# Kernel tuning notes

Measured on AMD Instinct MI355X. Metric: run time of the kernel, lower is better.

The kernel has to match this reference:

```python
import jax, jax.numpy as jnp
import numpy as np

E, TOPK, D, F, FS = 16, 4, 2560, 1664, 3328
B, S = 1, 2048


def setup_inputs() -> dict:
    key = jax.random.key(0)
    ks = jax.random.split(key, 8)
    sc = lambda *sh: 1.0 / np.sqrt(sh[-2] if len(sh) > 1 else 1.0)
    return {
        "hidden_states": jax.random.normal(ks[0], (B, S, D), jnp.float32),
        "router_weight": jax.random.normal(ks[1], (E, D), jnp.float32) * (1.0 / np.sqrt(D)),
        "w_gate": jax.random.normal(ks[2], (E, D, F), jnp.float32) * (1.0 / np.sqrt(D)),
        "w_up": jax.random.normal(ks[3], (E, D, F), jnp.float32) * (1.0 / np.sqrt(D)),
        "w_down": jax.random.normal(ks[4], (E, F, D), jnp.float32) * (1.0 / np.sqrt(F)),
        "sw_gate": jax.random.normal(ks[5], (D, FS), jnp.float32) * (1.0 / np.sqrt(D)),
        "sw_up": jax.random.normal(ks[6], (D, FS), jnp.float32) * (1.0 / np.sqrt(D)),
        "sw_down": jax.random.normal(ks[7], (FS, D), jnp.float32) * (1.0 / np.sqrt(FS)),
    }


def reference(hidden_states, router_weight, w_gate, w_up, w_down, sw_gate, sw_up, sw_down):
    b, s, d = hidden_states.shape
    x = hidden_states.reshape(-1, d)  # [T, D]
    T = x.shape[0]

    # Router: linear -> softmax -> top-k -> renormalize (vLLM FusedMoE default)
    logits = x @ router_weight.T                      # [T, E]
    probs = jax.nn.softmax(logits, axis=-1)
    topk_w, topk_idx = jax.lax.top_k(probs, TOPK)     # [T, K]
    topk_w = topk_w / jnp.sum(topk_w, axis=-1, keepdims=True)
    combine = jnp.zeros((T, E), x.dtype).at[jnp.arange(T)[:, None], topk_idx].add(topk_w)  # [T, E]

    # Expert SiLU-gated MLPs (dense-dispatch reference for grouped GEMM)
    g = jnp.einsum('td,edf->tef', x, w_gate)          # [T, E, F]
    u = jnp.einsum('td,edf->tef', x, w_up)
    h = jax.nn.silu(g) * u
    y = jnp.einsum('tef,efd->ted', h, w_down)         # [T, E, D]
    sparse_out = jnp.einsum('ted,te->td', y, combine)

    # Shared expert: LlamaMLP with silu gate, no bias
    shared_out = (jax.nn.silu(x @ sw_gate) * (x @ sw_up)) @ sw_down

    return (sparse_out + shared_out).reshape(b, s, d)
```

## Files before the change

kernel.cpp:

```cpp
#include <hip/hip_runtime.h>
#include <hip/hip_bf16.h>
#include <stdint.h>

#define E_N 16
#define TOPK 4
#define DD 2560
#define FF 1664
#define FSS 3328
#define TT 2048

typedef __attribute__((ext_vector_type(8))) __bf16 bf16x8;
typedef __attribute__((ext_vector_type(4))) float f32x4;

__device__ __forceinline__ unsigned short f2bf(float f) {
  return __builtin_bit_cast(unsigned short, (__bf16)f);
}
__device__ __forceinline__ float bf2f(unsigned short u) {
  return __builtin_bit_cast(float, (unsigned int)u << 16);
}
__device__ __forceinline__ unsigned int pk2(float a, float b) {
  return (unsigned int)f2bf(a) | ((unsigned int)f2bf(b) << 16);
}

#define GLOAD16(g, l)                                                          \
  __builtin_amdgcn_global_load_lds(                                            \
      (const __attribute__((address_space(1))) void*)(g),                      \
      (__attribute__((address_space(3))) void*)(l), 16, 0, 0)

#define SBAR() __builtin_amdgcn_s_barrier()
#define VMW(N) asm volatile("s_waitcnt vmcnt(" #N ")" ::: "memory")

__device__ __forceinline__ void swz_block(int& bm, int& bn, int& bz) {
  int gx = gridDim.x, gy = gridDim.y;
  int nwg = gx * gy * gridDim.z;
  int flat = blockIdx.x + gx * (blockIdx.y + gy * blockIdx.z);
  if ((nwg & 7) == 0) flat = (flat & 7) * (nwg >> 3) + (flat >> 3);
  bm = flat % gx;
  int rest = flat / gx;
  bn = rest % gy;
  bz = rest / gy;
}

__global__ __launch_bounds__(256) void cvt_bf16_kernel(const float* __restrict__ in,
                                                       unsigned short* __restrict__ out) {
  size_t i = ((size_t)blockIdx.x * 256 + threadIdx.x) * 4;
  float4 v = *reinterpret_cast<const float4*>(in + i);
  ushort4 o;
  o.x = f2bf(v.x); o.y = f2bf(v.y); o.z = f2bf(v.z); o.w = f2bf(v.w);
  *reinterpret_cast<ushort4*>(out + i) = o;
}

__global__ __launch_bounds__(256) void tcvt_kernel(const float* __restrict__ in,
                                                   unsigned short* __restrict__ out,
                                                   int K, int N) {
  __shared__ float lds[64 * 65];
  int z = blockIdx.z;
  in += (size_t)z * K * N;
  out += (size_t)z * K * N;
  int k0 = blockIdx.x * 64, n0 = blockIdx.y * 64;
  int t = threadIdx.x;
#pragma unroll
  for (int j = 0; j < 4; ++j) {
    int idx = j * 256 + t;
    int r = idx >> 4, c = (idx & 15) * 4;
    float4 v = *reinterpret_cast<const float4*>(in + (size_t)(k0 + r) * N + n0 + c);
    lds[r * 65 + c] = v.x;
    lds[r * 65 + c + 1] = v.y;
    lds[r * 65 + c + 2] = v.z;
    lds[r * 65 + c + 3] = v.w;
  }
  __syncthreads();
#pragma unroll
  for (int j = 0; j < 2; ++j) {
    int idx = j * 256 + t;
    int n = idx >> 3, kg = (idx & 7) * 8;
    float a0 = lds[(kg + 0) * 65 + n], a1 = lds[(kg + 1) * 65 + n];
    float a2 = lds[(kg + 2) * 65 + n], a3 = lds[(kg + 3) * 65 + n];
    float a4 = lds[(kg + 4) * 65 + n], a5 = lds[(kg + 5) * 65 + n];
    float a6 = lds[(kg + 6) * 65 + n], a7 = lds[(kg + 7) * 65 + n];
    uint4 o{pk2(a0, a1), pk2(a2, a3), pk2(a4, a5), pk2(a6, a7)};
    *reinterpret_cast<uint4*>(out + (size_t)(n0 + n) * K + k0 + kg) = o;
  }
}

__global__ __launch_bounds__(256) void router_kernel(const float* __restrict__ x,
                                                     const float* __restrict__ rw,
                                                     int* __restrict__ cnt,
                                                     int* __restrict__ list,
                                                     float* __restrict__ tw) {
  int t = blockIdx.x;
  const float* xr = x + (size_t)t * DD;
  __shared__ float logits[E_N];
  int lane = threadIdx.x & 63, wid = threadIdx.x >> 6;
  for (int ee = 0; ee < 4; ++ee) {
    int e = wid * 4 + ee;
    const float* wr = rw + (size_t)e * DD;
    float p = 0.f;
    for (int d = lane; d < DD; d += 64) p += xr[d] * wr[d];
#pragma unroll
    for (int off = 32; off > 0; off >>= 1) p += __shfl_down(p, off);
    if (lane == 0) logits[e] = p;
  }
  __syncthreads();
  if (threadIdx.x == 0) {
    float mx = -1e30f;
    for (int e = 0; e < E_N; ++e) mx = fmaxf(mx, logits[e]);
    float pe[E_N];
    for (int e = 0; e < E_N; ++e) pe[e] = __expf(logits[e] - mx);
    int idx[TOPK]; float val[TOPK]; float s4 = 0.f;
    unsigned used = 0;
    for (int k = 0; k < TOPK; ++k) {
      int bi = 0; float bv = -1.f;
      for (int e = 0; e < E_N; ++e)
        if (!((used >> e) & 1) && pe[e] > bv) { bv = pe[e]; bi = e; }
      used |= 1u << bi; idx[k] = bi; val[k] = bv; s4 += bv;
    }
    float inv = 1.f / s4;
    for (int k = 0; k < TOPK; ++k) {
      int e2 = idx[k];
      int pos = atomicAdd(&cnt[e2], 1);
      list[e2 * TT + pos] = t * 4 + k;
      tw[t * 4 + k] = val[k] * inv;
    }
  }
}

template <int MODE, int SHIFT>
__device__ __forceinline__ void gemm256(
    const unsigned short* __restrict__ A0, const unsigned short* __restrict__ W0,
    void* __restrict__ O0, const int* lst, const float* __restrict__ tw,
    int M, int Kt, int Nt, int m0, int n0) {
  __shared__ __align__(16) unsigned short lds[2][32768];

  int tid = threadIdx.x, lane = tid & 63, w = tid >> 6;
  int wm = w >> 2, wn = w & 3;

  const unsigned short* pA[2];
  const unsigned short* pB[2];
#pragma unroll
  for (int j = 0; j < 2; ++j) {
    int id = j * 512 + tid;
    int row = id >> 2, c = id & 3;
    int cs = c ^ ((row >> 1) & 3);
    int ar = min(m0 + row, M - 1);
    int code = lst ? lst[ar] : ar;
    int arow = SHIFT ? (lst ? (code >> 2) : code) : code;
    pA[j] = A0 + (size_t)arow * Kt + cs * 8;
    int br = min(n0 + row, Nt - 1);
    pB[j] = W0 + (size_t)br * Kt + cs * 8;
  }

  auto stage = [&](int kt, int h, int buf) {
    int koff = kt * 64 + h * 32;
    unsigned short* dA = &lds[buf][h * 8192];
    unsigned short* dB = &lds[buf][16384 + h * 8192];
#pragma unroll
    for (int j = 0; j < 2; ++j) {
      GLOAD16(pA[j] + koff, dA + (j * 512 + tid) * 8);
      GLOAD16(pB[j] + koff, dB + (j * 512 + tid) * 8);
    }
  };

  int cg = lane >> 4;
  int aoff[8], boff[4];
#pragma unroll
  for (int mf = 0; mf < 8; ++mf) {
    int r = wm * 128 + mf * 16 + (lane & 15);
    aoff[mf] = r * 32 + ((cg ^ ((r >> 1) & 3)) * 8);
  }
#pragma unroll
  for (int nf = 0; nf < 4; ++nf) {
    int rb = wn * 64 + nf * 16 + (lane & 15);
    boff[nf] = 16384 + rb * 32 + ((cg ^ ((rb >> 1) & 3)) * 8);
  }

  f32x4 acc[8][4] = {};

  auto half_compute = [&](int buf, int h) {
    const unsigned short* L = &lds[buf][h * 8192];
    bf16x8 a[8], b[4];
#pragma unroll
    for (int nf = 0; nf < 4; ++nf)
      b[nf] = __builtin_bit_cast(bf16x8, *reinterpret_cast<const uint4*>(L + boff[nf]));
#pragma unroll
    for (int mf = 0; mf < 8; ++mf)
      a[mf] = __builtin_bit_cast(bf16x8, *reinterpret_cast<const uint4*>(L + aoff[mf]));
    __builtin_amdgcn_s_setprio(1);
#pragma unroll
    for (int mf = 0; mf < 8; ++mf)
#pragma unroll
      for (int nf = 0; nf < 4; ++nf)
        acc[mf][nf] = __builtin_amdgcn_mfma_f32_16x16x32_bf16(a[mf], b[nf], acc[mf][nf], 0, 0, 0);
    __builtin_amdgcn_s_setprio(0);
  };

  int nk = Kt / 64;
  stage(0, 0, 0);
  stage(0, 1, 0);
  stage(1, 0, 1);
  for (int kt = 0; kt < nk; ++kt) {
    int buf = kt & 1;
    if (kt + 1 < nk) { VMW(8); } else { VMW(4); }
    SBAR();
    if (kt + 1 < nk) stage(kt + 1, 1, buf ^ 1);
    half_compute(buf, 0);
    if (kt + 1 < nk) { VMW(8); } else { VMW(0); }
    SBAR();
    if (kt + 2 < nk) stage(kt + 2, 0, buf);
    half_compute(buf, 1);
  }

#pragma unroll
  for (int mf = 0; mf < 8; ++mf) {
#pragma unroll
    for (int q = 0; q < 4; ++q) {
      int lr = wm * 128 + mf * 16 + (lane >> 4) * 4 + q;
      int grow = m0 + lr;
      if (grow < M) {
        int code = lst ? lst[grow] : grow;
        int col = n0 + wn * 64 + (lane & 15);
        if (MODE == 0) {
          unsigned short* Op = (unsigned short*)O0 + (size_t)code * Nt + col;
#pragma unroll
          for (int nf = 0; nf < 4; ++nf)
            if (col + nf * 16 < Nt) Op[nf * 16] = f2bf(acc[mf][nf][q]);
        } else {
          float scale = tw ? tw[code] : 1.f;
          float* Op = (float*)O0 + (size_t)code * Nt + col;
#pragma unroll
          for (int nf = 0; nf < 4; ++nf)
            if (col + nf * 16 < Nt) Op[nf * 16] = acc[mf][nf][q] * scale;
        }
      }
    }
  }
}

__global__ __launch_bounds__(512, 1) void gu256_kernel(
    const unsigned short* __restrict__ Xb,
    const unsigned short* __restrict__ WgT, const unsigned short* __restrict__ WuT,
    const unsigned short* __restrict__ SgT, const unsigned short* __restrict__ SuT,
    unsigned short* __restrict__ Gx, unsigned short* __restrict__ Ux,
    unsigned short* __restrict__ Gs, unsigned short* __restrict__ Us,
    const int* __restrict__ list, const int* __restrict__ cnt) {
  int bm, bn, z;
  swz_block(bm, bn, z);
  bool up = z >= 17;
  int ze = up ? z - 17 : z;
  const unsigned short* W0;
  unsigned short* O0;
  const int* lst = nullptr;
  int M, Nt;
  if (ze < E_N) {
    M = cnt[ze];
    lst = list + ze * TT;
    Nt = FF;
    W0 = (up ? WuT : WgT) + (size_t)ze * DD * FF;
    O0 = up ? Ux : Gx;
  } else {
    M = TT;
    Nt = FSS;
    W0 = up ? SuT : SgT;
    O0 = up ? Us : Gs;
  }
  int m0 = bm * 256, n0 = bn * 256;
  if (m0 >= M || n0 >= Nt) return;
  gemm256<0, 1>(Xb, W0, O0, lst, nullptr, M, DD, Nt, m0, n0);
}

__global__ __launch_bounds__(512, 1) void dn256_kernel(
    const unsigned short* __restrict__ Hx, const unsigned short* __restrict__ Hs,
    const unsigned short* __restrict__ WdT, const unsigned short* __restrict__ SdT,
    float* __restrict__ Y, float* __restrict__ Ys,
    const int* __restrict__ list, const int* __restrict__ cnt,
    const float* __restrict__ tw) {
  int bm, bn, z;
  swz_block(bm, bn, z);
  const unsigned short* A0;
  const unsigned short* W0;
  float* O0;
  const int* lst = nullptr;
  const float* sc = nullptr;
  int M, Kt;
  if (z < E_N) {
    M = cnt[z];
    lst = list + z * TT;
    Kt = FF;
    A0 = Hx;
    W0 = WdT + (size_t)z * FF * DD;
    O0 = Y;
    sc = tw;
  } else {
    M = TT;
    Kt = FSS;
    A0 = Hs;
    W0 = SdT;
    O0 = Ys;
  }
  int m0 = bm * 256, n0 = bn * 256;
  if (m0 >= M) return;
  gemm256<1, 0>(A0, W0, O0, lst, sc, M, Kt, DD, m0, n0);
}

__global__ __launch_bounds__(256) void h_kernel(const unsigned short* __restrict__ g,
                                                unsigned short* __restrict__ u) {
  size_t i = ((size_t)blockIdx.x * 256 + threadIdx.x) * 8;
  uint4 gv = *reinterpret_cast<const uint4*>(g + i);
  uint4 uv = *reinterpret_cast<const uint4*>(u + i);
  const unsigned int* gw = reinterpret_cast<const unsigned int*>(&gv);
  const unsigned int* uw = reinterpret_cast<const unsigned int*>(&uv);
  uint4 ov;
  unsigned int* ow = reinterpret_cast<unsigned int*>(&ov);
#pragma unroll
  for (int j = 0; j < 4; ++j) {
    float g0 = bf2f((unsigned short)(gw[j] & 0xffff));
    float g1 = bf2f((unsigned short)(gw[j] >> 16));
    float u0 = bf2f((unsigned short)(uw[j] & 0xffff));
    float u1 = bf2f((unsigned short)(uw[j] >> 16));
    float h0 = (g0 / (1.f + __expf(-g0))) * u0;
    float h1 = (g1 / (1.f + __expf(-g1))) * u1;
    ow[j] = pk2(h0, h1);
  }
  *reinterpret_cast<uint4*>(u + i) = ov;
}

__global__ __launch_bounds__(256) void combine_kernel(const float* __restrict__ Y,
                                                      const float* __restrict__ Ys,
                                                      float* __restrict__ out) {
  size_t i = ((size_t)blockIdx.x * 256 + threadIdx.x) * 4;
  size_t t = i / DD;
  int d = (int)(i % DD);
  float4 a = *reinterpret_cast<const float4*>(Ys + i);
#pragma unroll
  for (int k = 0; k < 4; ++k) {
    float4 v = *reinterpret_cast<const float4*>(Y + (t * 4 + k) * (size_t)DD + d);
    a.x += v.x; a.y += v.y; a.z += v.z; a.w += v.w;
  }
  *reinterpret_cast<float4*>(out + i) = a;
}

extern "C" void kernel_launch(void* const* d_in, const int* in_sizes, int n_in,
                              void* d_out, int out_size, void* d_ws, size_t ws_size,
                              hipStream_t stream) {
  const float* x  = (const float*)d_in[0];
  const float* rw = (const float*)d_in[1];
  const float* wg = (const float*)d_in[2];
  const float* wu = (const float*)d_in[3];
  const float* wd = (const float*)d_in[4];
  const float* sg = (const float*)d_in[5];
  const float* su = (const float*)d_in[6];
  const float* sd = (const float*)d_in[7];
  float* out = (float*)d_out;

  char* ws = (char*)d_ws;
  size_t off = 0;
  auto alloc = [&](size_t bytes) {
    off = (off + 255) & ~(size_t)255;
    void* p = ws + off;
    off += bytes;
    return p;
  };
  unsigned short* W1 = (unsigned short*)alloc((size_t)E_N * FF * DD * 2);
  unsigned short* W2 = (unsigned short*)alloc((size_t)E_N * FF * DD * 2);
  unsigned short* W3 = (unsigned short*)alloc((size_t)FSS * DD * 2);
  unsigned short* W4 = (unsigned short*)alloc((size_t)FSS * DD * 2);
  unsigned short* Xb = (unsigned short*)alloc((size_t)TT * DD * 2);
  unsigned short* Gx = (unsigned short*)alloc((size_t)4 * TT * FF * 2);
  unsigned short* Hx = (unsigned short*)alloc((size_t)4 * TT * FF * 2);
  unsigned short* Gs = (unsigned short*)alloc((size_t)TT * FSS * 2);
  unsigned short* Hs = (unsigned short*)alloc((size_t)TT * FSS * 2);
  float* Y  = (float*)alloc((size_t)4 * TT * DD * 4);
  float* Ys = (float*)alloc((size_t)TT * DD * 4);
  float* tw = (float*)alloc((size_t)4 * TT * 4);
  int* cnt  = (int*)alloc(E_N * 4);
  int* list = (int*)alloc((size_t)E_N * TT * 4);
  (void)ws_size; (void)in_sizes; (void)n_in; (void)out_size;

  hipMemsetAsync(cnt, 0, E_N * 4, stream);
  cvt_bf16_kernel<<<TT * DD / 4 / 256, 256, 0, stream>>>(x, Xb);
  router_kernel<<<TT, 256, 0, stream>>>(x, rw, cnt, list, tw);

  tcvt_kernel<<<dim3(DD / 64, FF / 64, E_N), 256, 0, stream>>>(wg, W1, DD, FF);
  tcvt_kernel<<<dim3(DD / 64, FF / 64, E_N), 256, 0, stream>>>(wu, W2, DD, FF);
  tcvt_kernel<<<dim3(DD / 64, FSS / 64, 1), 256, 0, stream>>>(sg, W3, DD, FSS);
  tcvt_kernel<<<dim3(DD / 64, FSS / 64, 1), 256, 0, stream>>>(su, W4, DD, FSS);

  gu256_kernel<<<dim3(TT / 256, (FSS + 255) / 256, 34), 512, 0, stream>>>(
      Xb, W1, W2, W3, W4, Gx, Hx, Gs, Hs, list, cnt);

  h_kernel<<<(size_t)4 * TT * FF / 8 / 256, 256, 0, stream>>>(Gx, Hx);
  h_kernel<<<(size_t)TT * FSS / 8 / 256, 256, 0, stream>>>(Gs, Hs);

  tcvt_kernel<<<dim3(FF / 64, DD / 64, E_N), 256, 0, stream>>>(wd, W1, FF, DD);
  tcvt_kernel<<<dim3(FSS / 64, DD / 64, 1), 256, 0, stream>>>(sd, W2, FSS, DD);

  dn256_kernel<<<dim3(TT / 256, DD / 256, 17), 512, 0, stream>>>(
      Hx, Hs, W1, W2, Y, Ys, list, cnt, tw);

  combine_kernel<<<TT * DD / 4 / 256, 256, 0, stream>>>(Y, Ys, out);
}
```

Baseline: 1.265 ms.

## Rework GEMM main loop into triple-buffered K=32 stages with split phases

Replaces the double-buffered K=64 LDS pipeline with a three-slot ring of K=32 tiles, prefetching two stages ahead. Each K step is split into two M-halves whose global loads are issued between the LDS reads and the MFMA burst. The goal is deeper latency hiding with smaller per-stage LDS use, at the cost of more barriers per K step and different wait-count logic. The grid y dimension is also changed from a ceiling division to an exact FSS/256, which gives the same value here.

```diff
diff --git a/kernel.cpp b/kernel.cpp
--- a/kernel.cpp
+++ b/kernel.cpp
@@ -126,117 +126,115 @@
 }
 
 template <int MODE, int SHIFT>
-__device__ __forceinline__ void gemm256(
+__device__ __forceinline__ void gemm8(
     const unsigned short* __restrict__ A0, const unsigned short* __restrict__ W0,
     void* __restrict__ O0, const int* lst, const float* __restrict__ tw,
     int M, int Kt, int Nt, int m0, int n0) {
-  __shared__ __align__(16) unsigned short lds[2][32768];
+  __shared__ __align__(16) unsigned short lds[3][16384];
 
   int tid = threadIdx.x, lane = tid & 63, w = tid >> 6;
   int wm = w >> 2, wn = w & 3;
 
+  int scs = (tid & 3) ^ ((tid >> 3) & 3);
   const unsigned short* pA[2];
   const unsigned short* pB[2];
 #pragma unroll
-  for (int j = 0; j < 2; ++j) {
-    int id = j * 512 + tid;
-    int row = id >> 2, c = id & 3;
-    int cs = c ^ ((row >> 1) & 3);
+  for (int h = 0; h < 2; ++h) {
+    int row = h * 128 + (tid >> 2);
     int ar = min(m0 + row, M - 1);
     int code = lst ? lst[ar] : ar;
     int arow = SHIFT ? (lst ? (code >> 2) : code) : code;
-    pA[j] = A0 + (size_t)arow * Kt + cs * 8;
+    pA[h] = A0 + (size_t)arow * Kt + scs * 8;
     int br = min(n0 + row, Nt - 1);
-    pB[j] = W0 + (size_t)br * Kt + cs * 8;
-  }
-
-  auto stage = [&](int kt, int h, int buf) {
-    int koff = kt * 64 + h * 32;
-    unsigned short* dA = &lds[buf][h * 8192];
-    unsigned short* dB = &lds[buf][16384 + h * 8192];
-#pragma unroll
-    for (int j = 0; j < 2; ++j) {
-      GLOAD16(pA[j] + koff, dA + (j * 512 + tid) * 8);
-      GLOAD16(pB[j] + koff, dB + (j * 512 + tid) * 8);
+    pB[h] = W0 + (size_t)br * Kt + scs * 8;
+  }
+
+  auto stage2 = [&](int kt, int h) {
+    unsigned short* d = &lds[kt % 3][0];
+    GLOAD16(pA[h] + kt * 32, d + h * 4096 + tid * 8);
+    GLOAD16(pB[h] + kt * 32, d + 8192 + h * 4096 + tid * 8);
+  };
+
+  int cg = lane >> 4;
+  int aoff[2][4], boff[4];
+#pragma unroll
+  for (int mq = 0; mq < 2; ++mq)
+#pragma unroll
+    for (int mf = 0; mf < 4; ++mf) {
+      int lr = mq * 64 + mf * 16 + (lane & 15);
+      aoff[mq][mf] = wm * 4096 + lr * 32 + ((cg ^ ((lr >> 1) & 3)) * 8);
     }
-  };
-
-  int cg = lane >> 4;
-  int aoff[8], boff[4];
-#pragma unroll
-  for (int mf = 0; mf < 8; ++mf) {
-    int r = wm * 128 + mf * 16 + (lane & 15);
-    aoff[mf] = r * 32 + ((cg ^ ((r >> 1) & 3)) * 8);
-  }
 #pragma unroll
   for (int nf = 0; nf < 4; ++nf) {
-    int rb = wn * 64 + nf * 16 + (lane & 15);
-    boff[nf] = 16384 + rb * 32 + ((cg ^ ((rb >> 1) & 3)) * 8);
+    int lr = (wn & 1) * 64 + nf * 16 + (lane & 15);
+    boff[nf] = 8192 + (wn >> 1) * 4096 + lr * 32 + ((cg ^ ((lr >> 1) & 3)) * 8);
   }
 
   f32x4 acc[8][4] = {};
 
-  auto half_compute = [&](int buf, int h) {
-    const unsigned short* L = &lds[buf][h * 8192];
-    bf16x8 a[8], b[4];
+  int nk = Kt / 32;
+  stage2(0, 0); stage2(0, 1);
+  stage2(1, 0); stage2(1, 1);
+  VMW(4);
+  SBAR();
+
+  for (int kt = 0; kt < nk; ++kt) {
+    const unsigned short* L = &lds[kt % 3][0];
+    bf16x8 b[4];
 #pragma unroll
     for (int nf = 0; nf < 4; ++nf)
       b[nf] = __builtin_bit_cast(bf16x8, *reinterpret_cast<const uint4*>(L + boff[nf]));
 #pragma unroll
-    for (int mf = 0; mf < 8; ++mf)
-      a[mf] = __builtin_bit_cast(bf16x8, *reinterpret_cast<const uint4*>(L + aoff[mf]));
-    __builtin_amdgcn_s_setprio(1);
-#pragma unroll
-    for (int mf = 0; mf < 8; ++mf)
-#pragma unroll
-      for (int nf = 0; nf < 4; ++nf)
-        acc[mf][nf] = __builtin_amdgcn_mfma_f32_16x16x32_bf16(a[mf], b[nf], acc[mf][nf], 0, 0, 0);
-    __builtin_amdgcn_s_setprio(0);
-  };
-
-  int nk = Kt / 64;
-  stage(0, 0, 0);
-  stage(0, 1, 0);
-  stage(1, 0, 1);
-  for (int kt = 0; kt < nk; ++kt) {
-    int buf = kt & 1;
-    if (kt + 1 < nk) { VMW(8); } else { VMW(4); }
-    SBAR();
-    if (kt + 1 < nk) stage(kt + 1, 1, buf ^ 1);
-    half_compute(buf, 0);
-    if (kt + 1 < nk) { VMW(8); } else { VMW(0); }
-    SBAR();
-    if (kt + 2 < nk) stage(kt + 2, 0, buf);
-    half_compute(buf, 1);
-  }
-
-#pragma unroll
-  for (int mf = 0; mf < 8; ++mf) {
-#pragma unroll
-    for (int q = 0; q < 4; ++q) {
-      int lr = wm * 128 + mf * 16 + (lane >> 4) * 4 + q;
-      int grow = m0 + lr;
-      if (grow < M) {
-        int code = lst ? lst[grow] : grow;
-        int col = n0 + wn * 64 + (lane & 15);
-        if (MODE == 0) {
-          unsigned short* Op = (unsigned short*)O0 + (size_t)code * Nt + col;
-#pragma unroll
-          for (int nf = 0; nf < 4; ++nf)
-            if (col + nf * 16 < Nt) Op[nf * 16] = f2bf(acc[mf][nf][q]);
-        } else {
-          float scale = tw ? tw[code] : 1.f;
-          float* Op = (float*)O0 + (size_t)code * Nt + col;
-#pragma unroll
-          for (int nf = 0; nf < 4; ++nf)
-            if (col + nf * 16 < Nt) Op[nf * 16] = acc[mf][nf][q] * scale;
+    for (int ph = 0; ph < 2; ++ph) {
+      bf16x8 a[4];
+#pragma unroll
+      for (int mf = 0; mf < 4; ++mf)
+        a[mf] = __builtin_bit_cast(bf16x8, *reinterpret_cast<const uint4*>(L + aoff[ph][mf]));
+      if (kt + 2 < nk) stage2(kt + 2, ph);
+      if (ph == 1) {
+        if (kt + 2 < nk) { VMW(4); }
+        else if (kt + 1 < nk) { VMW(0); }
+      }
+      SBAR();
+      __builtin_amdgcn_s_setprio(1);
+#pragma unroll
+      for (int mf = 0; mf < 4; ++mf)
+#pragma unroll
+        for (int nf = 0; nf < 4; ++nf)
+          acc[ph * 4 + mf][nf] = __builtin_amdgcn_mfma_f32_16x16x32_bf16(
+              a[mf], b[nf], acc[ph * 4 + mf][nf], 0, 0, 0);
+      __builtin_amdgcn_s_setprio(0);
+      SBAR();
+    }
+  }
+
+#pragma unroll
+  for (int mq = 0; mq < 2; ++mq)
+#pragma unroll
+    for (int mf = 0; mf < 4; ++mf)
+#pragma unroll
+      for (int q = 0; q < 4; ++q) {
+        int grow = m0 + wm * 128 + mq * 64 + mf * 16 + (lane >> 4) * 4 + q;
+        if (grow < M) {
+          int code = lst ? lst[grow] : grow;
+          int col = n0 + wn * 64 + (lane & 15);
+          if (MODE == 0) {
+            unsigned short* Op = (unsigned short*)O0 + (size_t)code * Nt + col;
+#pragma unroll
+            for (int nf = 0; nf < 4; ++nf)
+              if (col + nf * 16 < Nt) Op[nf * 16] = f2bf(acc[mq * 4 + mf][nf][q]);
+          } else {
+            float scale = tw ? tw[code] : 1.f;
+            float* Op = (float*)O0 + (size_t)code * Nt + col;
+#pragma unroll
+            for (int nf = 0; nf < 4; ++nf)
+              if (col + nf * 16 < Nt) Op[nf * 16] = acc[mq * 4 + mf][nf][q] * scale;
+          }
         }
       }
-    }
-  }
-}
-
-__global__ __launch_bounds__(512, 1) void gu256_kernel(
+}
+
+__global__ __launch_bounds__(512, 1) void gu8_kernel(
     const unsigned short* __restrict__ Xb,
     const unsigned short* __restrict__ WgT, const unsigned short* __restrict__ WuT,
     const unsigned short* __restrict__ SgT, const unsigned short* __restrict__ SuT,
@@ -265,10 +263,10 @@
   }
   int m0 = bm * 256, n0 = bn * 256;
   if (m0 >= M || n0 >= Nt) return;
-  gemm256<0, 1>(Xb, W0, O0, lst, nullptr, M, DD, Nt, m0, n0);
-}
-
-__global__ __launch_bounds__(512, 1) void dn256_kernel(
+  gemm8<0, 1>(Xb, W0, O0, lst, nullptr, M, DD, Nt, m0, n0);
+}
+
+__global__ __launch_bounds__(512, 1) void dn8_kernel(
     const unsigned short* __restrict__ Hx, const unsigned short* __restrict__ Hs,
     const unsigned short* __restrict__ WdT, const unsigned short* __restrict__ SdT,
     float* __restrict__ Y, float* __restrict__ Ys,
@@ -299,7 +297,7 @@
   }
   int m0 = bm * 256, n0 = bn * 256;
   if (m0 >= M) return;
-  gemm256<1, 0>(A0, W0, O0, lst, sc, M, Kt, DD, m0, n0);
+  gemm8<1, 0>(A0, W0, O0, lst, sc, M, Kt, DD, m0, n0);
 }
 
 __global__ __launch_bounds__(256) void h_kernel(const unsigned short* __restrict__ g,
@@ -385,7 +383,7 @@
   tcvt_kernel<<<dim3(DD / 64, FSS / 64, 1), 256, 0, stream>>>(sg, W3, DD, FSS);
   tcvt_kernel<<<dim3(DD / 64, FSS / 64, 1), 256, 0, stream>>>(su, W4, DD, FSS);
 
-  gu256_kernel<<<dim3(TT / 256, (FSS + 255) / 256, 34), 512, 0, stream>>>(
+  gu8_kernel<<<dim3(TT / 256, FSS / 256, 34), 512, 0, stream>>>(
       Xb, W1, W2, W3, W4, Gx, Hx, Gs, Hs, list, cnt);
 
   h_kernel<<<(size_t)4 * TT * FF / 8 / 256, 256, 0, stream>>>(Gx, Hx);
@@ -394,7 +392,7 @@
   tcvt_kernel<<<dim3(FF / 64, DD / 64, E_N), 256, 0, stream>>>(wd, W1, FF, DD);
   tcvt_kernel<<<dim3(FSS / 64, DD / 64, 1), 256, 0, stream>>>(sd, W2, FSS, DD);
 
-  dn256_kernel<<<dim3(TT / 256, DD / 256, 17), 512, 0, stream>>>(
+  dn8_kernel<<<dim3(TT / 256, DD / 256, 17), 512, 0, stream>>>(
       Hx, Hs, W1, W2, Y, Ys, list, cnt, tw);
 
   combine_kernel<<<TT * DD / 4 / 256, 256, 0, stream>>>(Y, Ys, out);
```

New measurement: 1.312 ms. 3.8% more time.

## Fuse gate/up GEMMs with SiLU epilogue and use 4-stage K pipeline

Applied to the files above, without the earlier changes.

Each block now loads a 128-column slice of both the gate and up weights into one B tile. SiLU(g)*u is computed in the epilogue and H is written directly. This removes the separate G/U intermediate buffers and the two elementwise h_kernel launches, along with their global-memory round trip. Both GEMMs also move from a two-buffer, two-half-step K=64 loop to a four-buffer K=32 ring with three stages in flight. The launch grid's x dimension grows to TT*4/256, so many blocks exit immediately, which adds some launch overhead.

```diff
diff --git a/kernel.cpp b/kernel.cpp
--- a/kernel.cpp
+++ b/kernel.cpp
@@ -15,9 +15,6 @@
 __device__ __forceinline__ unsigned short f2bf(float f) {
   return __builtin_bit_cast(unsigned short, (__bf16)f);
 }
-__device__ __forceinline__ float bf2f(unsigned short u) {
-  return __builtin_bit_cast(float, (unsigned int)u << 16);
-}
 __device__ __forceinline__ unsigned int pk2(float a, float b) {
   return (unsigned int)f2bf(a) | ((unsigned int)f2bf(b) << 16);
 }
@@ -29,6 +26,7 @@
 
 #define SBAR() __builtin_amdgcn_s_barrier()
 #define VMW(N) asm volatile("s_waitcnt vmcnt(" #N ")" ::: "memory")
+#define LGKM0() asm volatile("s_waitcnt lgkmcnt(0)" ::: "memory")
 
 __device__ __forceinline__ void swz_block(int& bm, int& bn, int& bz) {
   int gx = gridDim.x, gy = gridDim.y;
@@ -125,12 +123,28 @@
   }
 }
 
-template <int MODE, int SHIFT>
-__device__ __forceinline__ void gemm256(
-    const unsigned short* __restrict__ A0, const unsigned short* __restrict__ W0,
-    void* __restrict__ O0, const int* lst, const float* __restrict__ tw,
-    int M, int Kt, int Nt, int m0, int n0) {
-  __shared__ __align__(16) unsigned short lds[2][32768];
+__global__ __launch_bounds__(512, 1) void guF_kernel(
+    const unsigned short* __restrict__ Xb,
+    const unsigned short* __restrict__ WgT, const unsigned short* __restrict__ WuT,
+    const unsigned short* __restrict__ SgT, const unsigned short* __restrict__ SuT,
+    unsigned short* __restrict__ Hx, unsigned short* __restrict__ Hs,
+    const int* __restrict__ list, const int* __restrict__ cnt) {
+  int bm, bn, z;
+  swz_block(bm, bn, z);
+  const unsigned short *G0, *U0;
+  unsigned short* O0;
+  const int* lst = nullptr;
+  int M, Nt;
+  if (z < E_N) {
+    M = cnt[z]; lst = list + z * TT; Nt = FF;
+    G0 = WgT + (size_t)z * DD * FF; U0 = WuT + (size_t)z * DD * FF; O0 = Hx;
+  } else {
+    M = TT; Nt = FSS; G0 = SgT; U0 = SuT; O0 = Hs;
+  }
+  int m0 = bm * 256, n0 = bn * 128;
+  if (m0 >= M || n0 >= Nt) return;
+
+  __shared__ __align__(16) unsigned short lds[4][16384];
 
   int tid = threadIdx.x, lane = tid & 63, w = tid >> 6;
   int wm = w >> 2, wn = w & 3;
@@ -144,20 +158,19 @@
     int cs = c ^ ((row >> 1) & 3);
     int ar = min(m0 + row, M - 1);
     int code = lst ? lst[ar] : ar;
-    int arow = SHIFT ? (lst ? (code >> 2) : code) : code;
-    pA[j] = A0 + (size_t)arow * Kt + cs * 8;
-    int br = min(n0 + row, Nt - 1);
-    pB[j] = W0 + (size_t)br * Kt + cs * 8;
-  }
-
-  auto stage = [&](int kt, int h, int buf) {
-    int koff = kt * 64 + h * 32;
-    unsigned short* dA = &lds[buf][h * 8192];
-    unsigned short* dB = &lds[buf][16384 + h * 8192];
+    int tok = lst ? (code >> 2) : code;
+    pA[j] = Xb + (size_t)tok * DD + cs * 8;
+    pB[j] = (row < 128) ? (G0 + (size_t)(n0 + row) * DD + cs * 8)
+                        : (U0 + (size_t)(n0 + row - 128) * DD + cs * 8);
+  }
+
+  auto stage = [&](int kt) {
+    unsigned short* d = &lds[kt & 3][0];
+    int ko = kt * 32;
 #pragma unroll
     for (int j = 0; j < 2; ++j) {
-      GLOAD16(pA[j] + koff, dA + (j * 512 + tid) * 8);
-      GLOAD16(pB[j] + koff, dB + (j * 512 + tid) * 8);
+      GLOAD16(pA[j] + ko, d + (j * 512 + tid) * 8);
+      GLOAD16(pB[j] + ko, d + 8192 + (j * 512 + tid) * 8);
     }
   };
 
@@ -170,14 +183,21 @@
   }
 #pragma unroll
   for (int nf = 0; nf < 4; ++nf) {
-    int rb = wn * 64 + nf * 16 + (lane & 15);
-    boff[nf] = 16384 + rb * 32 + ((cg ^ ((rb >> 1) & 3)) * 8);
+    int r = (nf < 2 ? 0 : 128) + wn * 32 + (nf & 1) * 16 + (lane & 15);
+    boff[nf] = 8192 + r * 32 + ((cg ^ ((r >> 1) & 3)) * 8);
   }
 
   f32x4 acc[8][4] = {};
 
-  auto half_compute = [&](int buf, int h) {
-    const unsigned short* L = &lds[buf][h * 8192];
+  int nk = DD / 32;
+  stage(0); stage(1); stage(2);
+  for (int kt = 0; kt < nk; ++kt) {
+    int rem = nk - 1 - kt;
+    if (rem >= 2) { VMW(8); } else if (rem == 1) { VMW(4); } else { VMW(0); }
+    LGKM0();
+    SBAR();
+    if (kt + 3 < nk) stage(kt + 3);
+    const unsigned short* L = &lds[kt & 3][0];
     bf16x8 a[8], b[4];
 #pragma unroll
     for (int nf = 0; nf < 4; ++nf)
@@ -192,83 +212,27 @@
       for (int nf = 0; nf < 4; ++nf)
         acc[mf][nf] = __builtin_amdgcn_mfma_f32_16x16x32_bf16(a[mf], b[nf], acc[mf][nf], 0, 0, 0);
     __builtin_amdgcn_s_setprio(0);
-  };
-
-  int nk = Kt / 64;
-  stage(0, 0, 0);
-  stage(0, 1, 0);
-  stage(1, 0, 1);
-  for (int kt = 0; kt < nk; ++kt) {
-    int buf = kt & 1;
-    if (kt + 1 < nk) { VMW(8); } else { VMW(4); }
-    SBAR();
-    if (kt + 1 < nk) stage(kt + 1, 1, buf ^ 1);
-    half_compute(buf, 0);
-    if (kt + 1 < nk) { VMW(8); } else { VMW(0); }
-    SBAR();
-    if (kt + 2 < nk) stage(kt + 2, 0, buf);
-    half_compute(buf, 1);
   }
 
 #pragma unroll
   for (int mf = 0; mf < 8; ++mf) {
 #pragma unroll
     for (int q = 0; q < 4; ++q) {
-      int lr = wm * 128 + mf * 16 + (lane >> 4) * 4 + q;
-      int grow = m0 + lr;
+      int grow = m0 + wm * 128 + mf * 16 + (lane >> 4) * 4 + q;
       if (grow < M) {
         int code = lst ? lst[grow] : grow;
-        int col = n0 + wn * 64 + (lane & 15);
-        if (MODE == 0) {
-          unsigned short* Op = (unsigned short*)O0 + (size_t)code * Nt + col;
-#pragma unroll
-          for (int nf = 0; nf < 4; ++nf)
-            if (col + nf * 16 < Nt) Op[nf * 16] = f2bf(acc[mf][nf][q]);
-        } else {
-          float scale = tw ? tw[code] : 1.f;
-          float* Op = (float*)O0 + (size_t)code * Nt + col;
-#pragma unroll
-          for (int nf = 0; nf < 4; ++nf)
-            if (col + nf * 16 < Nt) Op[nf * 16] = acc[mf][nf][q] * scale;
+        unsigned short* Op = O0 + (size_t)code * Nt + n0 + wn * 32 + (lane & 15);
+#pragma unroll
+        for (int j = 0; j < 2; ++j) {
+          float g = acc[mf][j][q], u = acc[mf][2 + j][q];
+          Op[j * 16] = f2bf((g / (1.f + __expf(-g))) * u);
         }
       }
     }
   }
 }
 
-__global__ __launch_bounds__(512, 1) void gu256_kernel(
-    const unsigned short* __restrict__ Xb,
-    const unsigned short* __restrict__ WgT, const unsigned short* __restrict__ WuT,
-    const unsigned short* __restrict__ SgT, const unsigned short* __restrict__ SuT,
-    unsigned short* __restrict__ Gx, unsigned short* __restrict__ Ux,
-    unsigned short* __restrict__ Gs, unsigned short* __restrict__ Us,
-    const int* __restrict__ list, const int* __restrict__ cnt) {
-  int bm, bn, z;
-  swz_block(bm, bn, z);
-  bool up = z >= 17;
-  int ze = up ? z - 17 : z;
-  const unsigned short* W0;
-  unsigned short* O0;
-  const int* lst = nullptr;
-  int M, Nt;
-  if (ze < E_N) {
-    M = cnt[ze];
-    lst = list + ze * TT;
-    Nt = FF;
-    W0 = (up ? WuT : WgT) + (size_t)ze * DD * FF;
-    O0 = up ? Ux : Gx;
-  } else {
-    M = TT;
-    Nt = FSS;
-    W0 = up ? SuT : SgT;
-    O0 = up ? Us : Gs;
-  }
-  int m0 = bm * 256, n0 = bn * 256;
-  if (m0 >= M || n0 >= Nt) return;
-  gemm256<0, 1>(Xb, W0, O0, lst, nullptr, M, DD, Nt, m0, n0);
-}
-
-__global__ __launch_bounds__(512, 1) void dn256_kernel(
+__global__ __launch_bounds__(512, 1) void dnF_kernel(
     const unsigned short* __restrict__ Hx, const unsigned short* __restrict__ Hs,
     const unsigned short* __restrict__ WdT, const unsigned short* __restrict__ SdT,
     float* __restrict__ Y, float* __restrict__ Ys,
@@ -283,45 +247,96 @@
   const float* sc = nullptr;
   int M, Kt;
   if (z < E_N) {
-    M = cnt[z];
-    lst = list + z * TT;
-    Kt = FF;
-    A0 = Hx;
-    W0 = WdT + (size_t)z * FF * DD;
-    O0 = Y;
-    sc = tw;
+    M = cnt[z]; lst = list + z * TT; Kt = FF;
+    A0 = Hx; W0 = WdT + (size_t)z * FF * DD; O0 = Y; sc = tw;
   } else {
-    M = TT;
-    Kt = FSS;
-    A0 = Hs;
-    W0 = SdT;
-    O0 = Ys;
+    M = TT; Kt = FSS; A0 = Hs; W0 = SdT; O0 = Ys;
   }
   int m0 = bm * 256, n0 = bn * 256;
   if (m0 >= M) return;
-  gemm256<1, 0>(A0, W0, O0, lst, sc, M, Kt, DD, m0, n0);
-}
-
-__global__ __launch_bounds__(256) void h_kernel(const unsigned short* __restrict__ g,
-                                                unsigned short* __restrict__ u) {
-  size_t i = ((size_t)blockIdx.x * 256 + threadIdx.x) * 8;
-  uint4 gv = *reinterpret_cast<const uint4*>(g + i);
-  uint4 uv = *reinterpret_cast<const uint4*>(u + i);
-  const unsigned int* gw = reinterpret_cast<const unsigned int*>(&gv);
-  const unsigned int* uw = reinterpret_cast<const unsigned int*>(&uv);
-  uint4 ov;
-  unsigned int* ow = reinterpret_cast<unsigned int*>(&ov);
-#pragma unroll
-  for (int j = 0; j < 4; ++j) {
-    float g0 = bf2f((unsigned short)(gw[j] & 0xffff));
-    float g1 = bf2f((unsigned short)(gw[j] >> 16));
-    float u0 = bf2f((unsigned short)(uw[j] & 0xffff));
-    float u1 = bf2f((unsigned short)(uw[j] >> 16));
-    float h0 = (g0 / (1.f + __expf(-g0))) * u0;
-    float h1 = (g1 / (1.f + __expf(-g1))) * u1;
-    ow[j] = pk2(h0, h1);
-  }
-  *reinterpret_cast<uint4*>(u + i) = ov;
+
+  __shared__ __align__(16) unsigned short lds[4][16384];
+
+  int tid = threadIdx.x, lane = tid & 63, w = tid >> 6;
+  int wm = w >> 2, wn = w & 3;
+
+  const unsigned short* pA[2];
+  const unsigned short* pB[2];
+#pragma unroll
+  for (int j = 0; j < 2; ++j) {
+    int id = j * 512 + tid;
+    int row = id >> 2, c = id & 3;
+    int cs = c ^ ((row >> 1) & 3);
+    int ar = min(m0 + row, M - 1);
+    int code = lst ? lst[ar] : ar;
+    pA[j] = A0 + (size_t)code * Kt + cs * 8;
+    pB[j] = W0 + (size_t)(n0 + row) * Kt + cs * 8;
+  }
+
+  auto stage = [&](int kt) {
+    unsigned short* d = &lds[kt & 3][0];
+    int ko = kt * 32;
+#pragma unroll
+    for (int j = 0; j < 2; ++j) {
+      GLOAD16(pA[j] + ko, d + (j * 512 + tid) * 8);
+      GLOAD16(pB[j] + ko, d + 8192 + (j * 512 + tid) * 8);
+    }
+  };
+
+  int cg = lane >> 4;
+  int aoff[8], boff[4];
+#pragma unroll
+  for (int mf = 0; mf < 8; ++mf) {
+    int r = wm * 128 + mf * 16 + (lane & 15);
+    aoff[mf] = r * 32 + ((cg ^ ((r >> 1) & 3)) * 8);
+  }
+#pragma unroll
+  for (int nf = 0; nf < 4; ++nf) {
+    int r = wn * 64 + nf * 16 + (lane & 15);
+    boff[nf] = 8192 + r * 32 + ((cg ^ ((r >> 1) & 3)) * 8);
+  }
+
+  f32x4 acc[8][4] = {};
+
+  int nk = Kt / 32;
+  stage(0); stage(1); stage(2);
+  for (int kt = 0; kt < nk; ++kt) {
+    int rem = nk - 1 - kt;
+    if (rem >= 2) { VMW(8); } else if (rem == 1) { VMW(4); } else { VMW(0); }
+    LGKM0();
+    SBAR();
+    if (kt + 3 < nk) stage(kt + 3);
+    const unsigned short* L = &lds[kt & 3][0];
+    bf16x8 a[8], b[4];
+#pragma unroll
+    for (int nf = 0; nf < 4; ++nf)
+      b[nf] = __builtin_bit_cast(bf16x8, *reinterpret_cast<const uint4*>(L + boff[nf]));
+#pragma unroll
+    for (int mf = 0; mf < 8; ++mf)
+      a[mf] = __builtin_bit_cast(bf16x8, *reinterpret_cast<const uint4*>(L + aoff[mf]));
+    __builtin_amdgcn_s_setprio(1);
+#pragma unroll
+    for (int mf = 0; mf < 8; ++mf)
+#pragma unroll
+      for (int nf = 0; nf < 4; ++nf)
+        acc[mf][nf] = __builtin_amdgcn_mfma_f32_16x16x32_bf16(a[mf], b[nf], acc[mf][nf], 0, 0, 0);
+    __builtin_amdgcn_s_setprio(0);
+  }
+
+#pragma unroll
+  for (int mf = 0; mf < 8; ++mf) {
+#pragma unroll
+    for (int q = 0; q < 4; ++q) {
+      int grow = m0 + wm * 128 + mf * 16 + (lane >> 4) * 4 + q;
+      if (grow < M) {
+        int code = lst ? lst[grow] : grow;
+        float scale = sc ? sc[code] : 1.f;
+        float* Op = O0 + (size_t)code * DD + n0 + wn * 64 + (lane & 15);
+#pragma unroll
+        for (int nf = 0; nf < 4; ++nf) Op[nf * 16] = acc[mf][nf][q] * scale;
+      }
+    }
+  }
 }
 
 __global__ __launch_bounds__(256) void combine_kernel(const float* __restrict__ Y,
@@ -365,9 +380,7 @@
   unsigned short* W3 = (unsigned short*)alloc((size_t)FSS * DD * 2);
   unsigned short* W4 = (unsigned short*)alloc((size_t)FSS * DD * 2);
   unsigned short* Xb = (unsigned short*)alloc((size_t)TT * DD * 2);
-  unsigned short* Gx = (unsigned short*)alloc((size_t)4 * TT * FF * 2);
   unsigned short* Hx = (unsigned short*)alloc((size_t)4 * TT * FF * 2);
-  unsigned short* Gs = (unsigned short*)alloc((size_t)TT * FSS * 2);
   unsigned short* Hs = (unsigned short*)alloc((size_t)TT * FSS * 2);
   float* Y  = (float*)alloc((size_t)4 * TT * DD * 4);
   float* Ys = (float*)alloc((size_t)TT * DD * 4);
@@ -385,16 +398,13 @@
   tcvt_kernel<<<dim3(DD / 64, FSS / 64, 1), 256, 0, stream>>>(sg, W3, DD, FSS);
   tcvt_kernel<<<dim3(DD / 64, FSS / 64, 1), 256, 0, stream>>>(su, W4, DD, FSS);
 
-  gu256_kernel<<<dim3(TT / 256, (FSS + 255) / 256, 34), 512, 0, stream>>>(
-      Xb, W1, W2, W3, W4, Gx, Hx, Gs, Hs, list, cnt);
-
-  h_kernel<<<(size_t)4 * TT * FF / 8 / 256, 256, 0, stream>>>(Gx, Hx);
-  h_kernel<<<(size_t)TT * FSS / 8 / 256, 256, 0, stream>>>(Gs, Hs);
+  guF_kernel<<<dim3(TT * 4 / 256, FSS / 128, E_N + 1), 512, 0, stream>>>(
+      Xb, W1, W2, W3, W4, Hx, Hs, list, cnt);
 
   tcvt_kernel<<<dim3(FF / 64, DD / 64, E_N), 256, 0, stream>>>(wd, W1, FF, DD);
   tcvt_kernel<<<dim3(FSS / 64, DD / 64, 1), 256, 0, stream>>>(sd, W2, FSS, DD);
 
-  dn256_kernel<<<dim3(TT / 256, DD / 256, 17), 512, 0, stream>>>(
+  dnF_kernel<<<dim3(TT * 4 / 256, DD / 256, E_N + 1), 512, 0, stream>>>(
       Hx, Hs, W1, W2, Y, Ys, list, cnt, tw);
 
   combine_kernel<<<TT * DD / 4 / 256, 256, 0, stream>>>(Y, Ys, out);
```

New measurement: 1.441 ms. 1.14x slower.
